# Kernel tuning notes

Measured on AMD Instinct MI355X. Metric: run time of the kernel, lower is better.

Reference implementation:

```python
import jax, jax.numpy as jnp
import numpy as np

N_NODES = 100000
N_EDGES = 1600000
D = 64


def setup_inputs() -> dict:
    key = jax.random.key(0)
    k1, k2, k3, k4 = jax.random.split(key, 4)
    x = jax.random.normal(k1, (N_NODES, D), dtype=jnp.float32)
    # glorot-uniform scale for Linear weight [out_dim, in_dim]
    stdv = np.sqrt(6.0 / (D + D)).astype(np.float32)
    W = jax.random.uniform(k2, (D, D), dtype=jnp.float32, minval=-stdv, maxval=stdv)
    bias = jnp.zeros((D,), dtype=jnp.float32)  # forward() uses a zero bias
    edge_index = jax.random.randint(k3, (2, N_EDGES), 0, N_NODES, dtype=jnp.int64)
    counts = jax.random.randint(k4, (N_NODES,), 0, 16, dtype=jnp.int64)
    out_edge_index = jnp.arange(N_EDGES, dtype=jnp.int64)
    return {"x": x, "W": W, "bias": bias, "edge_index": edge_index,
            "counts": counts, "out_edge_index": out_edge_index, "layer_i": 0}


def reference(x, W, bias, edge_index, counts, out_edge_index, layer_i):
    # GCN layer: y = x @ W^T; gather by source; scatter-sum by destination; add bias.
    # counts / out_edge_index / layer_i are layout hints for the fused CUDA kernel
    # (mygraph.gcn) and do not change the math.
    y = x @ W.T                              # [N, D_out]
    src = edge_index[0]                      # [E]
    dst = edge_index[1]                      # [E]
    msgs = y[src]                            # [E, D_out] edge gather
    out = jax.ops.segment_sum(msgs, dst, num_segments=x.shape[0])  # [N, D_out]
    return out + bias
```

## Files before the change

### kernel.cpp

```cpp
#include <hip/hip_runtime.h>


#define DIM 64
#define BN 64
#define BN_SHIFT 6
#define BN_MASK 63
#define NB_MAX 2048
#define PB 256
#define KMAX 8
#define BPB 8192
#define SLDS_CAP 1536
#define AGS 64

typedef __attribute__((ext_vector_type(8))) short short8;
typedef __attribute__((ext_vector_type(4))) float f32x4;

__device__ __forceinline__ unsigned short f32_to_bf16_rne(float f) {
    unsigned u = __float_as_uint(f);
    unsigned r = u + 0x7FFFu + ((u >> 16) & 1u);
    return (unsigned short)(r >> 16);
}

__device__ __forceinline__ void pk2(float a, float b, unsigned &ph, unsigned &pl) {
    unsigned ha = f32_to_bf16_rne(a);
    unsigned hb = f32_to_bf16_rne(b);
    ph = ha | (hb << 16);
    float fa = __uint_as_float(ha << 16);
    float fb = __uint_as_float(hb << 16);
    unsigned la = f32_to_bf16_rne(a - fa);
    unsigned lb = f32_to_bf16_rne(b - fb);
    pl = la | (lb << 16);
}

__device__ __forceinline__ f32x4 mfma16(uint4 a, uint4 b, f32x4 c) {
    return __builtin_amdgcn_mfma_f32_16x16x32_bf16(
        __builtin_bit_cast(short8, a), __builtin_bit_cast(short8, b), c, 0, 0, 0);
}

__global__ __launch_bounds__(1024) void prep_sort_kernel(
        const float* __restrict__ x, const int* __restrict__ ei,
        ushort4* __restrict__ xb4, int* __restrict__ binned,
        int* __restrict__ off, int E, int N, int nb, int total4) {
    __shared__ int h[NB_MAX];
    __shared__ int staged[BPB];
    __shared__ int wsum[16];
    const int t = threadIdx.x;
    const int bid = blockIdx.x;
    const int lane = t & 63;
    const int wid = t >> 6;

    for (int b = t; b < nb; b += 1024) h[b] = 0;
    __syncthreads();

    int es[KMAX], ds[KMAX];
    #pragma unroll
    for (int k = 0; k < KMAX; ++k) {
        int e = (k * PB + bid) * 1024 + t;
        if (e < E) {
            es[k] = ei[e];
            ds[k] = ei[E + e];
            atomicAdd(&h[ds[k] >> BN_SHIFT], 1);
        } else {
            ds[k] = -1;
        }
    }

    for (int i = bid * 1024 + t; i < total4; i += PB * 1024) {
        float4 v = ((const float4*)x)[i];
        ushort4 o;
        o.x = f32_to_bf16_rne(v.x); o.y = f32_to_bf16_rne(v.y);
        o.z = f32_to_bf16_rne(v.z); o.w = f32_to_bf16_rne(v.w);
        xb4[i] = o;
    }
    if (bid == 0 && t < 16) {
        ushort4 z; z.x = 0; z.y = 0; z.z = 0; z.w = 0;
        xb4[(size_t)N * 16 + t] = z;
    }
    __syncthreads();

    int c0 = (2 * t < nb) ? h[2 * t] : 0;
    int c1 = (2 * t + 1 < nb) ? h[2 * t + 1] : 0;
    int s = c0 + c1;
    int incl = s;
    #pragma unroll
    for (int d = 1; d < 64; d <<= 1) {
        int u = __shfl_up(incl, d, 64);
        if (lane >= d) incl += u;
    }
    if (lane == 63) wsum[wid] = incl;
    __syncthreads();
    int woff = 0, EB = 0;
    for (int w = 0; w < 16; ++w) {
        if (w < wid) woff += wsum[w];
        EB += wsum[w];
    }
    int excl = woff + incl - s;
    if (2 * t < nb)     h[2 * t]     = excl;
    if (2 * t + 1 < nb) h[2 * t + 1] = excl + c0;
    __syncthreads();

    for (int b = t; b <= nb; b += 1024) {
        int v = (b < nb) ? h[b] : EB;
        off[(size_t)b * PB + bid] = v;
    }
    __syncthreads();

    #pragma unroll
    for (int k = 0; k < KMAX; ++k) {
        if (ds[k] >= 0) {
            int p = atomicAdd(&h[ds[k] >> BN_SHIFT], 1);
            staged[p] = (es[k] << BN_SHIFT) | (ds[k] & BN_MASK);
        }
    }
    __syncthreads();

    for (int i = t; i < EB; i += 1024)
        binned[(size_t)bid * BPB + i] = staged[i];
}

__device__ __forceinline__ void acc8(float (&a)[8], const uint4& v) {
    a[0] += __uint_as_float(v.x << 16); a[1] += __uint_as_float(v.x & 0xFFFF0000u);
    a[2] += __uint_as_float(v.y << 16); a[3] += __uint_as_float(v.y & 0xFFFF0000u);
    a[4] += __uint_as_float(v.z << 16); a[5] += __uint_as_float(v.z & 0xFFFF0000u);
    a[6] += __uint_as_float(v.w << 16); a[7] += __uint_as_float(v.w & 0xFFFF0000u);
}

#define PACK_STORE(AR, ROW)                                                   \
    do {                                                                      \
        unsigned ph0, ph1, ph2, ph3, pl0, pl1, pl2, pl3;                      \
        pk2(AR[0], AR[1], ph0, pl0); pk2(AR[2], AR[3], ph1, pl1);             \
        pk2(AR[4], AR[5], ph2, pl2); pk2(AR[6], AR[7], ph3, pl3);             \
        const int dco = (lane & 7) << 3;                                      \
        if (lane < 8) {                                                       \
            uint4 v; v.x = ph0; v.y = ph1; v.z = ph2; v.w = ph3;              \
            *(uint4*)&aggh[(ROW) * AGS + dco] = v;                            \
        } else if (lane < 16) {                                               \
            uint4 v; v.x = pl0; v.y = pl1; v.z = pl2; v.w = pl3;              \
            *(uint4*)&aggl[(ROW) * AGS + dco] = v;                            \
        }                                                                     \
    } while (0)

__global__ __launch_bounds__(256) void sort_gather_kernel(
        const unsigned short* __restrict__ xh,
        const int* __restrict__ binned, const int* __restrict__ off,
        const float* __restrict__ W, const float* __restrict__ bias,
        float* __restrict__ out, int N) {
    __shared__ int cnt[BN];
    __shared__ int basel[BN + 1];
    __shared__ int slds[SLDS_CAP];
    __shared__ __align__(16) unsigned short aggh[BN * AGS];
    __shared__ __align__(16) unsigned short aggl[BN * AGS];

    const int t = threadIdx.x;
    const int g = blockIdx.x;
    const int lane = t & 63;
    const int wid = t >> 6;
    const int node0 = g << BN_SHIFT;

    const int s_  = off[(size_t)g * PB + t];
    const int e_  = off[(size_t)(g + 1) * PB + t];
    const int gb  = t * BPB + s_;
    const int l_  = e_ - s_;

    if (t < BN) cnt[t] = 0;
    __syncthreads();

    for (int j = 0; j < l_; ++j) {
        int v = binned[gb + j];
        atomicAdd(&cnt[v & BN_MASK], 1);
    }
    __syncthreads();

    if (t < BN) {
        int myv = cnt[t];
        int v = myv;
        #pragma unroll
        for (int d = 1; d < BN; d <<= 1) {
            int u = __shfl_up(v, d, 64);
            if (t >= d) v += u;
        }
        basel[t] = v - myv;
        if (t == BN - 1) basel[BN] = v;
        cnt[t] = v - myv;
    }
    __syncthreads();

    for (int j = 0; j < l_; ++j) {
        int v = binned[gb + j];
        int p = atomicAdd(&cnt[v & BN_MASK], 1);
        if (p < SLDS_CAP) slds[p] = v >> BN_SHIFT;
    }
    __syncthreads();

    const int sub8 = lane >> 3;
    const int fb   = (lane & 7) << 3;
    const int zrow = N;
    for (int q = wid; q < (BN >> 2); q += 4) {
        const int nl = q << 2;
        int b0 = basel[nl + 0], e0 = basel[nl + 1];
        int b1 = basel[nl + 1], e1 = basel[nl + 2];
        int b2 = basel[nl + 2], e2 = basel[nl + 3];
        int b3 = basel[nl + 3], e3 = basel[nl + 4];
        int c0 = (e0 - b0 + 7) >> 3, c1 = (e1 - b1 + 7) >> 3;
        int c2 = (e2 - b2 + 7) >> 3, c3 = (e3 - b3 + 7) >> 3;
        int cmax = max(max(c0, c1), max(c2, c3));
        cmax = __builtin_amdgcn_readfirstlane(cmax);

        float A0[8] = {0.f,0.f,0.f,0.f,0.f,0.f,0.f,0.f};
        float A1[8] = {0.f,0.f,0.f,0.f,0.f,0.f,0.f,0.f};
        float A2[8] = {0.f,0.f,0.f,0.f,0.f,0.f,0.f,0.f};
        float A3[8] = {0.f,0.f,0.f,0.f,0.f,0.f,0.f,0.f};

        for (int c = 0; c < cmax; ++c) {
            const int o = (c << 3) + sub8;
            int i0 = b0 + o, i1 = b1 + o, i2 = b2 + o, i3 = b3 + o;
            int s0 = slds[min(i0, SLDS_CAP - 1)];
            int s1 = slds[min(i1, SLDS_CAP - 1)];
            int s2 = slds[min(i2, SLDS_CAP - 1)];
            int s3 = slds[min(i3, SLDS_CAP - 1)];
            s0 = (i0 < e0) ? s0 : zrow;
            s1 = (i1 < e1) ? s1 : zrow;
            s2 = (i2 < e2) ? s2 : zrow;
            s3 = (i3 < e3) ? s3 : zrow;
            uint4 v0 = *(const uint4*)(xh + (size_t)s0 * DIM + fb);
            uint4 v1 = *(const uint4*)(xh + (size_t)s1 * DIM + fb);
            uint4 v2 = *(const uint4*)(xh + (size_t)s2 * DIM + fb);
            uint4 v3 = *(const uint4*)(xh + (size_t)s3 * DIM + fb);
            acc8(A0, v0); acc8(A1, v1); acc8(A2, v2); acc8(A3, v3);
        }

        #pragma unroll
        for (int d = 8; d <= 32; d <<= 1) {
            #pragma unroll
            for (int j = 0; j < 8; ++j) {
                A0[j] += __shfl_xor(A0[j], d, 64);
                A1[j] += __shfl_xor(A1[j], d, 64);
                A2[j] += __shfl_xor(A2[j], d, 64);
                A3[j] += __shfl_xor(A3[j], d, 64);
            }
        }

        PACK_STORE(A0, nl + 0);
        PACK_STORE(A1, nl + 1);
        PACK_STORE(A2, nl + 2);
        PACK_STORE(A3, nl + 3);
    }

    __syncthreads();

    {
        const int mbase = wid << 4;
        const int l15 = lane & 15;
        const int kq  = lane >> 4;

        const unsigned short* arow_h = aggh + (mbase + l15) * AGS + (kq << 3);
        const unsigned short* arow_l = aggl + (mbase + l15) * AGS + (kq << 3);
        uint4 ah0 = *(const uint4*)(arow_h);
        uint4 ah1 = *(const uint4*)(arow_h + 32);
        uint4 al0 = *(const uint4*)(arow_l);
        uint4 al1 = *(const uint4*)(arow_l + 32);

        f32x4 acc[4];
        #pragma unroll
        for (int n = 0; n < 4; ++n) {
            float bb = bias[(n << 4) + l15];
            acc[n] = (f32x4){bb, bb, bb, bb};
        }

        #pragma unroll
        for (int n = 0; n < 4; ++n) {
            const float* wr = W + (size_t)((n << 4) + l15) * DIM + (kq << 3);
            float4 wa = *(const float4*)(wr);
            float4 wb = *(const float4*)(wr + 4);
            float4 wc = *(const float4*)(wr + 32);
            float4 wd = *(const float4*)(wr + 36);
            uint4 bh0, bl0, bh1, bl1;
            pk2(wa.x, wa.y, bh0.x, bl0.x); pk2(wa.z, wa.w, bh0.y, bl0.y);
            pk2(wb.x, wb.y, bh0.z, bl0.z); pk2(wb.z, wb.w, bh0.w, bl0.w);
            pk2(wc.x, wc.y, bh1.x, bl1.x); pk2(wc.z, wc.w, bh1.y, bl1.y);
            pk2(wd.x, wd.y, bh1.z, bl1.z); pk2(wd.z, wd.w, bh1.w, bl1.w);
            acc[n] = mfma16(ah0, bh0, acc[n]);
            acc[n] = mfma16(al0, bh0, acc[n]);
            acc[n] = mfma16(ah0, bl0, acc[n]);
            acc[n] = mfma16(ah1, bh1, acc[n]);
            acc[n] = mfma16(al1, bh1, acc[n]);
            acc[n] = mfma16(ah1, bl1, acc[n]);
        }

        #pragma unroll
        for (int n = 0; n < 4; ++n) {
            #pragma unroll
            for (int i = 0; i < 4; ++i) {
                int node = node0 + mbase + (kq << 2) + i;
                if (node < N)
                    out[(size_t)node * DIM + (n << 4) + l15] = acc[n][i];
            }
        }
    }
}

__global__ void gcn_scatter_kernel(const float* __restrict__ x,
                                   const int* __restrict__ edge_index,
                                   float* __restrict__ out, int n_edges) {
    int gid = blockIdx.x * blockDim.x + threadIdx.x;
    int e = gid >> 4;
    if (e >= n_edges) return;
    int j = (gid & 15) << 2;
    int src = edge_index[e];
    int dst = edge_index[n_edges + e];
    const float4 v = *(const float4*)(x + (size_t)src * DIM + j);
    float* o = out + (size_t)dst * DIM + j;
    atomicAdd(o + 0, v.x); atomicAdd(o + 1, v.y);
    atomicAdd(o + 2, v.z); atomicAdd(o + 3, v.w);
}

__global__ void gcn_linear_inplace_kernel(float* __restrict__ out,
                                          const float* __restrict__ W,
                                          const float* __restrict__ bias,
                                          int n_nodes) {
    __shared__ float Wt[DIM * DIM];
    __shared__ float rows[4][DIM];
    int tid = threadIdx.x;
    int col = tid & 63;
    int r = tid >> 6;
    for (int i = tid; i < DIM * DIM; i += 256) {
        int c = i >> 6, k = i & 63;
        Wt[k * DIM + c] = W[i];
    }
    int row = blockIdx.x * 4 + r;
    if (row < n_nodes) rows[r][col] = out[(size_t)row * DIM + col];
    __syncthreads();
    if (row < n_nodes) {
        float a = 0.f;
        #pragma unroll
        for (int k = 0; k < DIM; ++k) a += rows[r][k] * Wt[k * DIM + col];
        out[(size_t)row * DIM + col] = a + bias[col];
    }
}

extern "C" void kernel_launch(void* const* d_in, const int* in_sizes, int n_in,
                              void* d_out, int out_size, void* d_ws, size_t ws_size,
                              hipStream_t stream) {
    const float* x          = (const float*)d_in[0];
    const float* W          = (const float*)d_in[1];
    const float* bias       = (const float*)d_in[2];
    const int*   edge_index = (const int*)d_in[3];

    const int E = in_sizes[3] / 2;
    const int N = in_sizes[0] / DIM;
    float* out = (float*)d_out;

    const int nb = (N + BN - 1) >> BN_SHIFT;

    auto align256 = [](size_t v) { return (v + 255) & ~(size_t)255; };
    const size_t xb_b  = align256(((size_t)N + 1) * DIM * 2);
    const size_t bin_b = align256((size_t)PB * BPB * 4);
    const size_t off_b = align256(((size_t)nb + 1) * PB * 4);
    const size_t need  = xb_b + bin_b + off_b;

    if (nb < NB_MAX && N < (1 << 24) && ws_size >= need &&
        (long long)E <= (long long)PB * 1024 * KMAX) {
        char* p = (char*)d_ws;
        ushort4* xb4 = (ushort4*)p;          p += xb_b;
        int* binned  = (int*)p;              p += bin_b;
        int* off     = (int*)p;

        const int total4 = N * DIM / 4;

        prep_sort_kernel<<<PB, 1024, 0, stream>>>(
            x, edge_index, xb4, binned, off, E, N, nb, total4);
        sort_gather_kernel<<<nb, 256, 0, stream>>>(
            (const unsigned short*)xb4, binned, off, W, bias, out, N);
    } else {
        hipMemsetAsync(d_out, 0, (size_t)out_size * sizeof(float), stream);
        long long total = (long long)E * 16;
        int grid = (int)((total + 255) / 256);
        gcn_scatter_kernel<<<grid, 256, 0, stream>>>(x, edge_index, out, E);
        int lgrid = (N + 3) / 4;
        gcn_linear_inplace_kernel<<<lgrid, 256, 0, stream>>>(out, W, bias, N);
    }
}
```

Measured before the change: 176.1 us.

## Merge four node bins per block with coalesced LDS staging and 512 threads

Each workgroup now handles 256 nodes (four 64-node bins) with 512 threads. It first copies each producer's binned entries into a contiguous LDS raw buffer, tagging each with its sub-bin, using a prefix sum over segment lengths. It then runs the counting sort from LDS instead of walking global memory serially per thread twice. The aim is to cut the serial per-thread global loops and the per-block setup overhead, and to raise parallelism. In exchange it needs much more LDS (about 40KB or more), which may lower occupancy, and the 64-node aggregation plus MFMA stage becomes a sequential chunk loop with extra barriers.

```diff
diff --git a/kernel.cpp b/kernel.cpp
--- a/kernel.cpp
+++ b/kernel.cpp
@@ -9,8 +9,9 @@
 #define PB 256
 #define KMAX 8
 #define BPB 8192
-#define SLDS_CAP 1536
+#define RAW4 5120
 #define AGS 64
+#define SBN 256
 
 typedef __attribute__((ext_vector_type(8))) short short8;
 typedef __attribute__((ext_vector_type(4))) float f32x4;
@@ -140,162 +141,221 @@
         }                                                                     \
     } while (0)
 
-__global__ __launch_bounds__(256) void sort_gather_kernel(
+__global__ __launch_bounds__(512) void sort_gather_kernel(
         const unsigned short* __restrict__ xh,
         const int* __restrict__ binned, const int* __restrict__ off,
         const float* __restrict__ W, const float* __restrict__ bias,
-        float* __restrict__ out, int N) {
-    __shared__ int cnt[BN];
-    __shared__ int basel[BN + 1];
-    __shared__ int slds[SLDS_CAP];
-    __shared__ __align__(16) unsigned short aggh[BN * AGS];
-    __shared__ __align__(16) unsigned short aggl[BN * AGS];
+        float* __restrict__ out, int N, int nb) {
+    __shared__ int cnt[SBN];
+    __shared__ int basel[SBN + 1];
+    __shared__ int wsum[8];
+    __shared__ int sbase[PB], slen[PB], sgb[PB];
+    __shared__ int sb1[PB], sb2[PB], sb3[PB];
+    __shared__ int slds[RAW4];
+    __shared__ __align__(16) int uni[RAW4];
+
+    int* raw = uni;
+    unsigned short* aggh = (unsigned short*)uni;
+    unsigned short* aggl = (unsigned short*)(uni + 2048);
 
     const int t = threadIdx.x;
     const int g = blockIdx.x;
     const int lane = t & 63;
     const int wid = t >> 6;
-    const int node0 = g << BN_SHIFT;
-
-    const int s_  = off[(size_t)g * PB + t];
-    const int e_  = off[(size_t)(g + 1) * PB + t];
-    const int gb  = t * BPB + s_;
-    const int l_  = e_ - s_;
-
-    if (t < BN) cnt[t] = 0;
-    __syncthreads();
-
-    for (int j = 0; j < l_; ++j) {
-        int v = binned[gb + j];
-        atomicAdd(&cnt[v & BN_MASK], 1);
-    }
-    __syncthreads();
-
-    if (t < BN) {
-        int myv = cnt[t];
-        int v = myv;
-        #pragma unroll
-        for (int d = 1; d < BN; d <<= 1) {
-            int u = __shfl_up(v, d, 64);
-            if (t >= d) v += u;
+    const int node0 = g << 8;
+
+    if (t < PB) {
+        int lo = min(4 * g,     nb);
+        int r1 = min(4 * g + 1, nb);
+        int r2 = min(4 * g + 2, nb);
+        int r3 = min(4 * g + 3, nb);
+        int hi = min(4 * g + 4, nb);
+        int s_ = off[(size_t)lo * PB + t];
+        int e_ = off[(size_t)hi * PB + t];
+        slen[t] = e_ - s_;
+        sgb[t]  = t * BPB + s_;
+        sb1[t]  = off[(size_t)r1 * PB + t] - s_;
+        sb2[t]  = off[(size_t)r2 * PB + t] - s_;
+        sb3[t]  = off[(size_t)r3 * PB + t] - s_;
+    }
+    if (t < SBN) cnt[t] = 0;
+    __syncthreads();
+
+    int myl = (t < PB) ? slen[t] : 0;
+    int v = myl;
+    #pragma unroll
+    for (int d = 1; d < 64; d <<= 1) {
+        int u = __shfl_up(v, d, 64);
+        if (lane >= d) v += u;
+    }
+    if (lane == 63 && wid < 4) wsum[wid] = v;
+    __syncthreads();
+    int total = wsum[0] + wsum[1] + wsum[2] + wsum[3];
+    if (t < PB) {
+        int w0 = 0;
+        for (int w = 0; w < wid; ++w) w0 += wsum[w];
+        sbase[t] = w0 + v - myl;
+    }
+    __syncthreads();
+    const int tot = min(total, RAW4);
+
+    {
+        const int tt = t & (PB - 1);
+        const int half = t >> 8;
+        const int ls = slen[tt];
+        const int bs = sbase[tt];
+        const int gbs = sgb[tt];
+        const int B1 = sb1[tt], B2 = sb2[tt], B3 = sb3[tt];
+        for (int j = half; j < ls; j += 2) {
+            int w = binned[gbs + j];
+            int sub = (j >= B3) ? 3 : ((j >= B2) ? 2 : ((j >= B1) ? 1 : 0));
+            int p = bs + j;
+            if (p < RAW4)
+                raw[p] = ((w >> BN_SHIFT) << 8) | (sub << 6) | (w & BN_MASK);
         }
-        basel[t] = v - myv;
-        if (t == BN - 1) basel[BN] = v;
-        cnt[t] = v - myv;
-    }
-    __syncthreads();
-
-    for (int j = 0; j < l_; ++j) {
-        int v = binned[gb + j];
-        int p = atomicAdd(&cnt[v & BN_MASK], 1);
-        if (p < SLDS_CAP) slds[p] = v >> BN_SHIFT;
+    }
+    __syncthreads();
+
+    for (int i = t; i < tot; i += 512)
+        atomicAdd(&cnt[raw[i] & 255], 1);
+    __syncthreads();
+
+    int myv = (t < SBN) ? cnt[t] : 0;
+    int iv = myv;
+    #pragma unroll
+    for (int d = 1; d < 64; d <<= 1) {
+        int u = __shfl_up(iv, d, 64);
+        if (lane >= d) iv += u;
+    }
+    if (lane == 63 && wid < 4) wsum[wid] = iv;
+    __syncthreads();
+    if (t < SBN) {
+        int w0 = 0;
+        for (int w = 0; w < wid; ++w) w0 += wsum[w];
+        int excl = w0 + iv - myv;
+        basel[t] = excl;
+        cnt[t] = excl;
+    }
+    if (t == 0) basel[SBN] = tot;
+    __syncthreads();
+
+    for (int i = t; i < tot; i += 512) {
+        int w = raw[i];
+        int p = atomicAdd(&cnt[w & 255], 1);
+        slds[p] = w >> 8;
     }
     __syncthreads();
 
     const int sub8 = lane >> 3;
     const int fb   = (lane & 7) << 3;
     const int zrow = N;
-    for (int q = wid; q < (BN >> 2); q += 4) {
-        const int nl = q << 2;
-        int b0 = basel[nl + 0], e0 = basel[nl + 1];
-        int b1 = basel[nl + 1], e1 = basel[nl + 2];
-        int b2 = basel[nl + 2], e2 = basel[nl + 3];
-        int b3 = basel[nl + 3], e3 = basel[nl + 4];
-        int c0 = (e0 - b0 + 7) >> 3, c1 = (e1 - b1 + 7) >> 3;
-        int c2 = (e2 - b2 + 7) >> 3, c3 = (e3 - b3 + 7) >> 3;
-        int cmax = max(max(c0, c1), max(c2, c3));
-        cmax = __builtin_amdgcn_readfirstlane(cmax);
-
-        float A0[8] = {0.f,0.f,0.f,0.f,0.f,0.f,0.f,0.f};
-        float A1[8] = {0.f,0.f,0.f,0.f,0.f,0.f,0.f,0.f};
-        float A2[8] = {0.f,0.f,0.f,0.f,0.f,0.f,0.f,0.f};
-        float A3[8] = {0.f,0.f,0.f,0.f,0.f,0.f,0.f,0.f};
-
-        for (int c = 0; c < cmax; ++c) {
-            const int o = (c << 3) + sub8;
-            int i0 = b0 + o, i1 = b1 + o, i2 = b2 + o, i3 = b3 + o;
-            int s0 = slds[min(i0, SLDS_CAP - 1)];
-            int s1 = slds[min(i1, SLDS_CAP - 1)];
-            int s2 = slds[min(i2, SLDS_CAP - 1)];
-            int s3 = slds[min(i3, SLDS_CAP - 1)];
-            s0 = (i0 < e0) ? s0 : zrow;
-            s1 = (i1 < e1) ? s1 : zrow;
-            s2 = (i2 < e2) ? s2 : zrow;
-            s3 = (i3 < e3) ? s3 : zrow;
-            uint4 v0 = *(const uint4*)(xh + (size_t)s0 * DIM + fb);
-            uint4 v1 = *(const uint4*)(xh + (size_t)s1 * DIM + fb);
-            uint4 v2 = *(const uint4*)(xh + (size_t)s2 * DIM + fb);
-            uint4 v3 = *(const uint4*)(xh + (size_t)s3 * DIM + fb);
-            acc8(A0, v0); acc8(A1, v1); acc8(A2, v2); acc8(A3, v3);
+    const int l15 = lane & 15;
+    const int kq  = lane >> 4;
+
+    for (int ch = 0; ch < 4; ++ch) {
+        const int nbase = ch << 6;
+
+        for (int q = wid; q < 16; q += 8) {
+            const int nl = nbase + (q << 2);
+            int b0 = basel[nl + 0], e0 = basel[nl + 1];
+            int b1 = basel[nl + 1], e1 = basel[nl + 2];
+            int b2 = basel[nl + 2], e2 = basel[nl + 3];
+            int b3 = basel[nl + 3], e3 = basel[nl + 4];
+            int c0 = (e0 - b0 + 7) >> 3, c1 = (e1 - b1 + 7) >> 3;
+            int c2 = (e2 - b2 + 7) >> 3, c3 = (e3 - b3 + 7) >> 3;
+            int cmax = max(max(c0, c1), max(c2, c3));
+            cmax = __builtin_amdgcn_readfirstlane(cmax);
+
+            float A0[8] = {0.f,0.f,0.f,0.f,0.f,0.f,0.f,0.f};
+            float A1[8] = {0.f,0.f,0.f,0.f,0.f,0.f,0.f,0.f};
+            float A2[8] = {0.f,0.f,0.f,0.f,0.f,0.f,0.f,0.f};
+            float A3[8] = {0.f,0.f,0.f,0.f,0.f,0.f,0.f,0.f};
+
+            for (int c = 0; c < cmax; ++c) {
+                const int o = (c << 3) + sub8;
+                int i0 = b0 + o, i1 = b1 + o, i2 = b2 + o, i3 = b3 + o;
+                int s0 = slds[min(i0, RAW4 - 1)];
+                int s1 = slds[min(i1, RAW4 - 1)];
+                int s2 = slds[min(i2, RAW4 - 1)];
+                int s3 = slds[min(i3, RAW4 - 1)];
+                s0 = (i0 < e0) ? s0 : zrow;
+                s1 = (i1 < e1) ? s1 : zrow;
+                s2 = (i2 < e2) ? s2 : zrow;
+                s3 = (i3 < e3) ? s3 : zrow;
+                uint4 v0 = *(const uint4*)(xh + (size_t)s0 * DIM + fb);
+                uint4 v1 = *(const uint4*)(xh + (size_t)s1 * DIM + fb);
+                uint4 v2 = *(const uint4*)(xh + (size_t)s2 * DIM + fb);
+                uint4 v3 = *(const uint4*)(xh + (size_t)s3 * DIM + fb);
+                acc8(A0, v0); acc8(A1, v1); acc8(A2, v2); acc8(A3, v3);
+            }
+
+            #pragma unroll
+            for (int d = 8; d <= 32; d <<= 1) {
+                #pragma unroll
+                for (int j = 0; j < 8; ++j) {
+                    A0[j] += __shfl_xor(A0[j], d, 64);
+                    A1[j] += __shfl_xor(A1[j], d, 64);
+                    A2[j] += __shfl_xor(A2[j], d, 64);
+                    A3[j] += __shfl_xor(A3[j], d, 64);
+                }
+            }
+
+            PACK_STORE(A0, (q << 2) + 0);
+            PACK_STORE(A1, (q << 2) + 1);
+            PACK_STORE(A2, (q << 2) + 2);
+            PACK_STORE(A3, (q << 2) + 3);
         }
 
-        #pragma unroll
-        for (int d = 8; d <= 32; d <<= 1) {
+        __syncthreads();
+
+        if (wid < 4) {
+            const int mbase = wid << 4;
+
+            const unsigned short* arow_h = aggh + (mbase + l15) * AGS + (kq << 3);
+            const unsigned short* arow_l = aggl + (mbase + l15) * AGS + (kq << 3);
+            uint4 ah0 = *(const uint4*)(arow_h);
+            uint4 ah1 = *(const uint4*)(arow_h + 32);
+            uint4 al0 = *(const uint4*)(arow_l);
+            uint4 al1 = *(const uint4*)(arow_l + 32);
+
+            f32x4 acc[4];
             #pragma unroll
-            for (int j = 0; j < 8; ++j) {
-                A0[j] += __shfl_xor(A0[j], d, 64);
-                A1[j] += __shfl_xor(A1[j], d, 64);
-                A2[j] += __shfl_xor(A2[j], d, 64);
-                A3[j] += __shfl_xor(A3[j], d, 64);
+            for (int n = 0; n < 4; ++n) {
+                float bb = bias[(n << 4) + l15];
+                acc[n] = (f32x4){bb, bb, bb, bb};
+            }
+
+            #pragma unroll
+            for (int n = 0; n < 4; ++n) {
+                const float* wr = W + (size_t)((n << 4) + l15) * DIM + (kq << 3);
+                float4 wa = *(const float4*)(wr);
+                float4 wb = *(const float4*)(wr + 4);
+                float4 wc = *(const float4*)(wr + 32);
+                float4 wd = *(const float4*)(wr + 36);
+                uint4 bh0, bl0, bh1, bl1;
+                pk2(wa.x, wa.y, bh0.x, bl0.x); pk2(wa.z, wa.w, bh0.y, bl0.y);
+                pk2(wb.x, wb.y, bh0.z, bl0.z); pk2(wb.z, wb.w, bh0.w, bl0.w);
+                pk2(wc.x, wc.y, bh1.x, bl1.x); pk2(wc.z, wc.w, bh1.y, bl1.y);
+                pk2(wd.x, wd.y, bh1.z, bl1.z); pk2(wd.z, wd.w, bh1.w, bl1.w);
+                acc[n] = mfma16(ah0, bh0, acc[n]);
+                acc[n] = mfma16(al0, bh0, acc[n]);
+                acc[n] = mfma16(ah0, bl0, acc[n]);
+                acc[n] = mfma16(ah1, bh1, acc[n]);
+                acc[n] = mfma16(al1, bh1, acc[n]);
+                acc[n] = mfma16(ah1, bl1, acc[n]);
+            }
+
+            #pragma unroll
+            for (int n = 0; n < 4; ++n) {
+                #pragma unroll
+                for (int i = 0; i < 4; ++i) {
+                    int node = node0 + nbase + mbase + (kq << 2) + i;
+                    if (node < N)
+                        out[(size_t)node * DIM + (n << 4) + l15] = acc[n][i];
+                }
             }
         }
-
-        PACK_STORE(A0, nl + 0);
-        PACK_STORE(A1, nl + 1);
-        PACK_STORE(A2, nl + 2);
-        PACK_STORE(A3, nl + 3);
-    }
-
-    __syncthreads();
-
-    {
-        const int mbase = wid << 4;
-        const int l15 = lane & 15;
-        const int kq  = lane >> 4;
-
-        const unsigned short* arow_h = aggh + (mbase + l15) * AGS + (kq << 3);
-        const unsigned short* arow_l = aggl + (mbase + l15) * AGS + (kq << 3);
-        uint4 ah0 = *(const uint4*)(arow_h);
-        uint4 ah1 = *(const uint4*)(arow_h + 32);
-        uint4 al0 = *(const uint4*)(arow_l);
-        uint4 al1 = *(const uint4*)(arow_l + 32);
-
-        f32x4 acc[4];
-        #pragma unroll
-        for (int n = 0; n < 4; ++n) {
-            float bb = bias[(n << 4) + l15];
-            acc[n] = (f32x4){bb, bb, bb, bb};
-        }
-
-        #pragma unroll
-        for (int n = 0; n < 4; ++n) {
-            const float* wr = W + (size_t)((n << 4) + l15) * DIM + (kq << 3);
-            float4 wa = *(const float4*)(wr);
-            float4 wb = *(const float4*)(wr + 4);
-            float4 wc = *(const float4*)(wr + 32);
-            float4 wd = *(const float4*)(wr + 36);
-            uint4 bh0, bl0, bh1, bl1;
-            pk2(wa.x, wa.y, bh0.x, bl0.x); pk2(wa.z, wa.w, bh0.y, bl0.y);
-            pk2(wb.x, wb.y, bh0.z, bl0.z); pk2(wb.z, wb.w, bh0.w, bl0.w);
-            pk2(wc.x, wc.y, bh1.x, bl1.x); pk2(wc.z, wc.w, bh1.y, bl1.y);
-            pk2(wd.x, wd.y, bh1.z, bl1.z); pk2(wd.z, wd.w, bh1.w, bl1.w);
-            acc[n] = mfma16(ah0, bh0, acc[n]);
-            acc[n] = mfma16(al0, bh0, acc[n]);
-            acc[n] = mfma16(ah0, bl0, acc[n]);
-            acc[n] = mfma16(ah1, bh1, acc[n]);
-            acc[n] = mfma16(al1, bh1, acc[n]);
-            acc[n] = mfma16(ah1, bl1, acc[n]);
-        }
-
-        #pragma unroll
-        for (int n = 0; n < 4; ++n) {
-            #pragma unroll
-            for (int i = 0; i < 4; ++i) {
-                int node = node0 + mbase + (kq << 2) + i;
-                if (node < N)
-                    out[(size_t)node * DIM + (n << 4) + l15] = acc[n][i];
-            }
-        }
+        __syncthreads();
     }
 }
 
@@ -350,7 +410,8 @@
     const int N = in_sizes[0] / DIM;
     float* out = (float*)d_out;
 
-    const int nb = (N + BN - 1) >> BN_SHIFT;
+    const int nb  = (N + BN - 1) >> BN_SHIFT;
+    const int nbg = (nb + 3) >> 2;
 
     auto align256 = [](size_t v) { return (v + 255) & ~(size_t)255; };
     const size_t xb_b  = align256(((size_t)N + 1) * DIM * 2);
@@ -369,8 +430,8 @@
 
         prep_sort_kernel<<<PB, 1024, 0, stream>>>(
             x, edge_index, xb4, binned, off, E, N, nb, total4);
-        sort_gather_kernel<<<nb, 256, 0, stream>>>(
-            (const unsigned short*)xb4, binned, off, W, bias, out, N);
+        sort_gather_kernel<<<nbg, 512, 0, stream>>>(
+            (const unsigned short*)xb4, binned, off, W, bias, out, N, nb);
     } else {
         hipMemsetAsync(d_out, 0, (size_t)out_size * sizeof(float), stream);
         long long total = (long long)E * 16;
```

Result: slower. 182.2 us (+3.4%).

## Replace per-block offset table with global per-bucket atomic bins and overflow list

Applied to the files above, without the earlier changes.

The prep kernel now reserves space in a fixed-capacity global bin per destination bucket using an atomic counter, instead of writing per-block staged runs plus an offset table that the gather kernel had to walk serially per thread. The gather kernel reads a contiguous bin segment with strided coalesced loads rather than each thread looping over its own run. Edges beyond the bin capacity go to an overflow list, which each block scans after its main work and handles with a scalar matvec and atomic adds. This adds a memset, global atomics in prep, and a full overflow-list scan per block whenever overflow occurs.

```diff
diff --git a/kernel.cpp b/kernel.cpp
--- a/kernel.cpp
+++ b/kernel.cpp
@@ -9,7 +9,8 @@
 #define PB 256
 #define KMAX 8
 #define BPB 8192
-#define SLDS_CAP 1536
+#define CAPE 1536
+#define OVF_MAX 262144
 #define AGS 64
 
 typedef __attribute__((ext_vector_type(8))) short short8;
@@ -37,10 +38,11 @@
         __builtin_bit_cast(short8, a), __builtin_bit_cast(short8, b), c, 0, 0, 0);
 }
 
-__global__ __launch_bounds__(1024) void prep_sort_kernel(
+__global__ __launch_bounds__(1024) void prep_hybrid_kernel(
         const float* __restrict__ x, const int* __restrict__ ei,
-        ushort4* __restrict__ xb4, int* __restrict__ binned,
-        int* __restrict__ off, int E, int N, int nb, int total4) {
+        ushort4* __restrict__ xb4, int* __restrict__ gcnt,
+        int* __restrict__ binned, int* __restrict__ ovf,
+        int* __restrict__ ovfcnt, int E, int N, int nb, int total4) {
     __shared__ int h[NB_MAX];
     __shared__ int staged[BPB];
     __shared__ int wsum[16];
@@ -89,20 +91,13 @@
     }
     if (lane == 63) wsum[wid] = incl;
     __syncthreads();
-    int woff = 0, EB = 0;
-    for (int w = 0; w < 16; ++w) {
+    int woff = 0;
+    for (int w = 0; w < 16; ++w)
         if (w < wid) woff += wsum[w];
-        EB += wsum[w];
-    }
-    int excl = woff + incl - s;
-    if (2 * t < nb)     h[2 * t]     = excl;
-    if (2 * t + 1 < nb) h[2 * t + 1] = excl + c0;
-    __syncthreads();
-
-    for (int b = t; b <= nb; b += 1024) {
-        int v = (b < nb) ? h[b] : EB;
-        off[(size_t)b * PB + bid] = v;
-    }
+    const int exc0 = woff + incl - s;
+    const int exc1 = exc0 + c0;
+    if (2 * t < nb)     h[2 * t]     = exc0;
+    if (2 * t + 1 < nb) h[2 * t + 1] = exc1;
     __syncthreads();
 
     #pragma unroll
@@ -114,8 +109,28 @@
     }
     __syncthreads();
 
-    for (int i = t; i < EB; i += 1024)
-        binned[(size_t)bid * BPB + i] = staged[i];
+    #pragma unroll
+    for (int half = 0; half < 2; ++half) {
+        int b  = 2 * t + half;
+        int c  = half ? c1 : c0;
+        int st = half ? exc1 : exc0;
+        if (b < nb && c > 0) {
+            int base = atomicAdd(&gcnt[b], c);
+            for (int j = 0; j < c; ++j) {
+                int v = staged[st + j];
+                int p = base + j;
+                if (p < CAPE) {
+                    binned[(size_t)b * CAPE + p] = v;
+                } else {
+                    int q = atomicAdd(ovfcnt, 1);
+                    if (q < OVF_MAX) {
+                        ovf[2 * q] = v >> BN_SHIFT;
+                        ovf[2 * q + 1] = (b << BN_SHIFT) | (v & BN_MASK);
+                    }
+                }
+            }
+        }
+    }
 }
 
 __device__ __forceinline__ void acc8(float (&a)[8], const uint4& v) {
@@ -141,13 +156,14 @@
     } while (0)
 
 __global__ __launch_bounds__(256) void sort_gather_kernel(
-        const unsigned short* __restrict__ xh,
-        const int* __restrict__ binned, const int* __restrict__ off,
+        const unsigned short* __restrict__ xh, const float* __restrict__ xf,
+        const int* __restrict__ binned, const int* __restrict__ gcnt,
+        const int* __restrict__ ovf, const int* __restrict__ ovfcnt,
         const float* __restrict__ W, const float* __restrict__ bias,
         float* __restrict__ out, int N) {
     __shared__ int cnt[BN];
     __shared__ int basel[BN + 1];
-    __shared__ int slds[SLDS_CAP];
+    __shared__ int slds[CAPE];
     __shared__ __align__(16) unsigned short aggh[BN * AGS];
     __shared__ __align__(16) unsigned short aggl[BN * AGS];
 
@@ -157,18 +173,16 @@
     const int wid = t >> 6;
     const int node0 = g << BN_SHIFT;
 
-    const int s_  = off[(size_t)g * PB + t];
-    const int e_  = off[(size_t)(g + 1) * PB + t];
-    const int gb  = t * BPB + s_;
-    const int l_  = e_ - s_;
+    const int seg0 = g * CAPE;
+    int len = gcnt[g];
+    if (len > CAPE) len = CAPE;
+    const int seg1 = seg0 + len;
 
     if (t < BN) cnt[t] = 0;
     __syncthreads();
 
-    for (int j = 0; j < l_; ++j) {
-        int v = binned[gb + j];
-        atomicAdd(&cnt[v & BN_MASK], 1);
-    }
+    for (int i = seg0 + t; i < seg1; i += 256)
+        atomicAdd(&cnt[binned[i] & BN_MASK], 1);
     __syncthreads();
 
     if (t < BN) {
@@ -185,10 +199,10 @@
     }
     __syncthreads();
 
-    for (int j = 0; j < l_; ++j) {
-        int v = binned[gb + j];
+    for (int i = seg0 + t; i < seg1; i += 256) {
+        int v = binned[i];
         int p = atomicAdd(&cnt[v & BN_MASK], 1);
-        if (p < SLDS_CAP) slds[p] = v >> BN_SHIFT;
+        slds[p] = v >> BN_SHIFT;
     }
     __syncthreads();
 
@@ -214,10 +228,10 @@
         for (int c = 0; c < cmax; ++c) {
             const int o = (c << 3) + sub8;
             int i0 = b0 + o, i1 = b1 + o, i2 = b2 + o, i3 = b3 + o;
-            int s0 = slds[min(i0, SLDS_CAP - 1)];
-            int s1 = slds[min(i1, SLDS_CAP - 1)];
-            int s2 = slds[min(i2, SLDS_CAP - 1)];
-            int s3 = slds[min(i3, SLDS_CAP - 1)];
+            int s0 = slds[min(i0, CAPE - 1)];
+            int s1 = slds[min(i1, CAPE - 1)];
+            int s2 = slds[min(i2, CAPE - 1)];
+            int s3 = slds[min(i3, CAPE - 1)];
             s0 = (i0 < e0) ? s0 : zrow;
             s1 = (i1 < e1) ? s1 : zrow;
             s2 = (i2 < e2) ? s2 : zrow;
@@ -297,6 +311,28 @@
             }
         }
     }
+
+    __syncthreads();
+    int oc = *ovfcnt;
+    if (oc > 0) {
+        if (oc > OVF_MAX) oc = OVF_MAX;
+        for (int i = wid; i < oc; i += 4) {
+            int s = ovf[2 * i];
+            int d = ovf[2 * i + 1];
+            if ((d >> BN_SHIFT) == g) {
+                float v = xf[(size_t)s * DIM + lane];
+                float rr0 = 0.f, rr1 = 0.f, rr2 = 0.f, rr3 = 0.f;
+                #pragma unroll
+                for (int k = 0; k < DIM; k += 4) {
+                    rr0 += __int_as_float(__builtin_amdgcn_readlane(__float_as_int(v), k + 0)) * W[(size_t)lane * DIM + k + 0];
+                    rr1 += __int_as_float(__builtin_amdgcn_readlane(__float_as_int(v), k + 1)) * W[(size_t)lane * DIM + k + 1];
+                    rr2 += __int_as_float(__builtin_amdgcn_readlane(__float_as_int(v), k + 2)) * W[(size_t)lane * DIM + k + 2];
+                    rr3 += __int_as_float(__builtin_amdgcn_readlane(__float_as_int(v), k + 3)) * W[(size_t)lane * DIM + k + 3];
+                }
+                atomicAdd(&out[(size_t)d * DIM + lane], (rr0 + rr1) + (rr2 + rr3));
+            }
+        }
+    }
 }
 
 __global__ void gcn_scatter_kernel(const float* __restrict__ x,
@@ -354,23 +390,28 @@
 
     auto align256 = [](size_t v) { return (v + 255) & ~(size_t)255; };
     const size_t xb_b  = align256(((size_t)N + 1) * DIM * 2);
-    const size_t bin_b = align256((size_t)PB * BPB * 4);
-    const size_t off_b = align256(((size_t)nb + 1) * PB * 4);
-    const size_t need  = xb_b + bin_b + off_b;
+    const size_t bin_b = align256((size_t)nb * CAPE * 4);
+    const size_t cnt_b = align256(((size_t)nb + 64) * 4);
+    const size_t ovf_b = align256((size_t)OVF_MAX * 2 * 4);
+    const size_t need  = xb_b + bin_b + cnt_b + ovf_b;
 
     if (nb < NB_MAX && N < (1 << 24) && ws_size >= need &&
         (long long)E <= (long long)PB * 1024 * KMAX) {
         char* p = (char*)d_ws;
         ushort4* xb4 = (ushort4*)p;          p += xb_b;
         int* binned  = (int*)p;              p += bin_b;
-        int* off     = (int*)p;
+        int* gcnt    = (int*)p;              p += cnt_b;
+        int* ovf     = (int*)p;
+        int* ovfcnt  = gcnt + nb;
 
         const int total4 = N * DIM / 4;
 
-        prep_sort_kernel<<<PB, 1024, 0, stream>>>(
-            x, edge_index, xb4, binned, off, E, N, nb, total4);
+        hipMemsetAsync(gcnt, 0, cnt_b, stream);
+        prep_hybrid_kernel<<<PB, 1024, 0, stream>>>(
+            x, edge_index, xb4, gcnt, binned, ovf, ovfcnt, E, N, nb, total4);
         sort_gather_kernel<<<nb, 256, 0, stream>>>(
-            (const unsigned short*)xb4, binned, off, W, bias, out, N);
+            (const unsigned short*)xb4, x, binned, gcnt, ovf, ovfcnt,
+            W, bias, out, N);
     } else {
         hipMemsetAsync(d_out, 0, (size_t)out_size * sizeof(float), stream);
         long long total = (long long)E * 16;
```

Result: no change. 174.3 us (-1.1%).
